# Optimization experiments

Hardware: AMD Instinct MI355X
Metric: run time of the kernel (lower is better)

Reference implementation:

```python
import jax, jax.numpy as jnp
import numpy as np

ND1 = 8000   # block1 num dst nodes
ND2 = 4000   # block2 num dst nodes


def gat_layer(x_src, x_dst, src, dst, num_dst, W, a_src, a_dst, b, heads, ch):
    """PyG GATConv (bipartite tuple input, concat=True) in jax.
    x_src: [B,Ns,F], x_dst: [B,Nd,F]; src/dst: [E] int edge endpoints."""
    B = x_src.shape[0]
    h_s = jnp.einsum('bnf,fk->bnk', x_src, W).reshape(B, -1, heads, ch)  # [B,Ns,H,C]
    h_d = jnp.einsum('bnf,fk->bnk', x_dst, W).reshape(B, -1, heads, ch)  # [B,Nd,H,C]
    e_s = jnp.einsum('bnhc,hc->bnh', h_s, a_src)  # [B,Ns,H]
    e_d = jnp.einsum('bnhc,hc->bnh', h_d, a_dst)  # [B,Nd,H]
    alpha = jax.nn.leaky_relu(e_s[:, src] + e_d[:, dst], 0.2)  # [B,E,H]
    a = jnp.transpose(alpha, (1, 0, 2))  # [E,B,H] (segment ops reduce axis 0)
    amax = jax.ops.segment_max(a, dst, num_segments=num_dst)  # [Nd,B,H]
    ex = jnp.exp(a - amax[dst])
    den = jax.ops.segment_sum(ex, dst, num_segments=num_dst)
    w = ex / (den[dst] + 1e-16)  # edge softmax per (dst,batch,head)
    msg = jnp.transpose(h_s[:, src], (1, 0, 2, 3)) * w[..., None]  # [E,B,H,C]
    out = jax.ops.segment_sum(msg, dst, num_segments=num_dst)  # [Nd,B,H,C]
    out = jnp.transpose(out, (1, 0, 2, 3)).reshape(B, num_dst, heads * ch)
    return out + b


def setup_inputs() -> dict:
    key = jax.random.key(0)
    ks = jax.random.split(key, 16)
    B, N, F = 2, 20000, 128
    E1, E2 = 100000, 60000
    inp = {
        'x': jax.random.normal(ks[0], (B, N, F), jnp.float32),
        'n_id1': jax.random.randint(ks[1], (16000,), 0, N),
        'res_n_id1': jax.random.randint(ks[2], (ND1,), 0, 16000),
        'src1': jax.random.randint(ks[3], (E1,), 0, 16000),
        'dst1': jax.random.randint(ks[4], (E1,), 0, ND1),
        'res_n_id2': jax.random.randint(ks[5], (ND2,), 0, ND1),
        'src2': jax.random.randint(ks[6], (E2,), 0, ND1),
        'dst2': jax.random.randint(ks[7], (E2,), 0, ND2),
        'W1': jax.random.normal(ks[8], (F, 12 * 128), jnp.float32) * 0.05,
        'att_src1': jax.random.normal(ks[9], (12, 128), jnp.float32) * 0.1,
        'att_dst1': jax.random.normal(ks[10], (12, 128), jnp.float32) * 0.1,
        'bias1': jnp.zeros((12 * 128,), jnp.float32),
        'W2': jax.random.normal(ks[11], (12 * 128, 1), jnp.float32) * 0.05,
        'att_src2': jax.random.normal(ks[12], (1, 1), jnp.float32) * 0.1,
        'att_dst2': jax.random.normal(ks[13], (1, 1), jnp.float32) * 0.1,
        'bias2': jnp.zeros((1,), jnp.float32),
    }
    return inp


def reference(x, n_id1, res_n_id1, src1, dst1, res_n_id2, src2, dst2,
              W1, att_src1, att_dst1, bias1, W2, att_src2, att_dst2, bias2):
    # block 1
    xt = x[:, n_id1, :]                       # [B,16000,F]
    xd = xt[:, res_n_id1, :]                  # [B,8000,F]
    h = gat_layer(xt, xd, src1, dst1, ND1, W1, att_src1, att_dst1, bias1, 12, 128)
    h = jax.nn.relu(h)                        # [B,8000,1536]
    # block 2
    hd = h[:, res_n_id2, :]                   # [B,4000,1536]
    out = gat_layer(h, hd, src2, dst2, ND2, W2, att_src2, att_dst2, bias2, 1, 1)
    return out                                # [B,4000,1]
```

## Files before the change

### kernel.cpp

```cpp
#include <hip/hip_runtime.h>
#include <hip/hip_bf16.h>

#define B2      2
#define NX      20000
#define F_IN    128
#define NS1     16000
#define ND1     8000
#define E1      100000
#define ND2     4000
#define E2      60000
#define HEADS   12
#define CH      128
#define K1      1536
#define MROWS   (2*ND1)
#define CAP1    64
#define CAP2    64

typedef __bf16 bf16x8 __attribute__((ext_vector_type(8)));
typedef float  f32x4  __attribute__((ext_vector_type(4)));

static __device__ __forceinline__ float lrelu(float x) { return x > 0.f ? x : 0.2f * x; }

static __device__ __forceinline__ unsigned short f2bf(float f) {
    union { float f; unsigned u; } v; v.f = f;
    unsigned r = v.u + 0x7fffu + ((v.u >> 16) & 1u);
    return (unsigned short)(r >> 16);
}
static __device__ __forceinline__ float bf2f(unsigned short h) {
    union { unsigned u; float f; } v; v.u = ((unsigned)h) << 16;
    return v.f;
}

static __device__ __forceinline__ void gld16(const void* g, void* l) {
    __builtin_amdgcn_global_load_lds(
        (const __attribute__((address_space(1))) unsigned int*)g,
        (__attribute__((address_space(3))) unsigned int*)l, 16, 0, 0);
}

__global__ __launch_bounds__(256) void k_prep(const float* __restrict__ x,
                                              const int* __restrict__ n_id,
                                              const float* __restrict__ W,
                                              const float* __restrict__ asrc,
                                              const float* __restrict__ adst,
                                              unsigned short* __restrict__ xg,
                                              unsigned short* __restrict__ WT,
                                              unsigned short* __restrict__ wswd,
                                              int* __restrict__ dcnt,
                                              float* __restrict__ s2)
{
    const int bx = blockIdx.x;
    const int tid = threadIdx.x;
    if (bx < 4000) {
        int t = bx * 256 + tid;
        int row = t >> 5;
        int c4 = (t & 31) << 2;
        int b = row >= NS1 ? 1 : 0;
        int node = n_id[row - b * NS1];
        const float4 v = *reinterpret_cast<const float4*>(
            x + ((size_t)(b * NX + node)) * F_IN + c4);
        ushort4 o;
        o.x = f2bf(v.x); o.y = f2bf(v.y); o.z = f2bf(v.z); o.w = f2bf(v.w);
        *reinterpret_cast<ushort4*>(xg + (size_t)row * F_IN + c4) = o;
    } else if (bx < 4768) {
        int t = (bx - 4000) * 256 + tid;
        int k = t / K1;
        int n = t - k * K1;
        WT[(size_t)n * F_IN + k] = f2bf(W[t]);
    } else if (bx < 4784) {
        int t = (bx - 4768) * 256 + tid;
        int n = t >> 7;
        int c = t & 127;
        float acc = 0.f;
        if (n < 24) {
            int h = n < 12 ? n : n - 12;
            const float* att = (n < 12 ? asrc : adst) + h * CH;
            const float* wr = W + (size_t)c * K1 + h * CH;
            for (int j = 0; j < CH; ++j) acc += wr[j] * att[j];
        }
        wswd[(size_t)n * F_IN + c] = f2bf(acc);
    } else {
        int t = (bx - 4784) * 256 + tid;
        if (t < ND1 + ND2) dcnt[t] = 0;
        else if (t < ND1 + ND2 + MROWS) s2[t - (ND1 + ND2)] = 0.f;
    }
}

__global__ __launch_bounds__(256) void k_escore(const unsigned short* __restrict__ xg,
                                                const unsigned short* __restrict__ wswd,
                                                float* __restrict__ es,
                                                float* __restrict__ ed)
{
    const int tid = threadIdx.x;
    const int wave = tid >> 6, lane = tid & 63;
    const int l15 = lane & 15, l4 = lane >> 4;
    const int rt = blockIdx.x * 4 + wave;
    const int row0 = rt * 16;
    const unsigned short* Ap = xg + (size_t)(row0 + l15) * F_IN + l4 * 8;

    f32x4 acc[2] = {f32x4{0,0,0,0}, f32x4{0,0,0,0}};
#pragma unroll
    for (int kk = 0; kk < 4; ++kk) {
        bf16x8 a = *reinterpret_cast<const bf16x8*>(Ap + kk * 32);
#pragma unroll
        for (int c = 0; c < 2; ++c) {
            bf16x8 b = *reinterpret_cast<const bf16x8*>(
                wswd + (size_t)(c * 16 + l15) * F_IN + kk * 32 + l4 * 8);
            acc[c] = __builtin_amdgcn_mfma_f32_16x16x32_bf16(a, b, acc[c], 0, 0, 0);
        }
    }
#pragma unroll
    for (int c = 0; c < 2; ++c) {
        int col = c * 16 + l15;
#pragma unroll
        for (int r = 0; r < 4; ++r) {
            int row = row0 + l4 * 4 + r;
            float v = acc[c][r];
            if (col < 12)       es[(size_t)row * HEADS + col] = v;
            else if (col < 24)  ed[(size_t)row * HEADS + (col - 12)] = v;
        }
    }
}

__global__ void k_scatter2(const int* __restrict__ dst1, const int* __restrict__ src1,
                           const int* __restrict__ dst2, const int* __restrict__ src2,
                           const int* __restrict__ res1,
                           const float* __restrict__ es, const float* __restrict__ ed,
                           int* __restrict__ dcnt, unsigned* __restrict__ ew,
                           int* __restrict__ srcp2)
{
    int e = blockIdx.x * 256 + threadIdx.x;
    if (e < E1) {
        int d = dst1[e];
        int k = atomicAdd(&dcnt[d], 1);
        if (k < CAP1) {
            int s = src1[e];
            int rd = res1[d];
#pragma unroll
            for (int b = 0; b < 2; ++b) {
                const float* esp = es + ((size_t)(b * NS1 + s)) * HEADS;
                const float* edp = ed + ((size_t)(b * NS1 + rd)) * HEADS;
                unsigned w[6];
#pragma unroll
                for (int j = 0; j < 6; ++j) {
                    float w0 = __expf(lrelu(esp[2 * j] + edp[2 * j]));
                    float w1 = __expf(lrelu(esp[2 * j + 1] + edp[2 * j + 1]));
                    w[j] = (unsigned)f2bf(w0) | ((unsigned)f2bf(w1) << 16);
                }
                unsigned* rp = ew + ((size_t)b * ND1 * CAP1 + (size_t)d * CAP1 + k) * 8;
                *reinterpret_cast<uint4*>(rp) = make_uint4((unsigned)s, w[0], w[1], w[2]);
                *reinterpret_cast<uint4*>(rp + 4) = make_uint4(w[3], w[4], w[5], 0u);
            }
        }
    } else if (e < E1 + E2) {
        int ee = e - E1;
        int d = dst2[ee];
        int k = atomicAdd(&dcnt[ND1 + d], 1);
        if (k < CAP2) srcp2[d * CAP2 + k] = src2[ee];
    }
}

__global__ __launch_bounds__(256) void k_agg1(const unsigned short* __restrict__ xg,
                                              const unsigned* __restrict__ ew,
                                              const int* __restrict__ dcnt,
                                              unsigned short* __restrict__ agg)
{
    const int tid = threadIdx.x;
    const int wv = tid >> 6, lane = tid & 63;
    const int task = blockIdx.x * 4 + wv;
    const int b = task >= ND1 ? 1 : 0;
    const int i = task - b * ND1;
    const int c2 = lane * 2;

    const int deg = min(dcnt[i], CAP1);
    const uint4* eb = reinterpret_cast<const uint4*>(
        ew + ((size_t)b * ND1 * CAP1 + (size_t)i * CAP1) * 8);
    const unsigned short* xb = xg + (size_t)b * NS1 * F_IN + c2;

    float acc[24];
    float den[12];
#pragma unroll
    for (int r = 0; r < 24; ++r) acc[r] = 0.f;
#pragma unroll
    for (int h = 0; h < 12; ++h) den[h] = 0.f;

#pragma unroll 2
    for (int p = 0; p < deg; ++p) {
        uint4 r0 = eb[2 * p];
        uint4 r1 = eb[2 * p + 1];
        int se = (int)r0.x;
        unsigned xv = *reinterpret_cast<const unsigned*>(xb + (size_t)se * F_IN);
        float x0 = __uint_as_float(xv << 16);
        float x1 = __uint_as_float(xv & 0xffff0000u);
        unsigned wd[6] = {r0.y, r0.z, r0.w, r1.x, r1.y, r1.z};
#pragma unroll
        for (int j = 0; j < 6; ++j) {
            unsigned d = wd[j];
            float w0 = __uint_as_float(d << 16);
            float w1 = __uint_as_float(d & 0xffff0000u);
            acc[4 * j + 0] += w0 * x0; acc[4 * j + 1] += w0 * x1;
            acc[4 * j + 2] += w1 * x0; acc[4 * j + 3] += w1 * x1;
            den[2 * j]     += w0;      den[2 * j + 1] += w1;
        }
    }

    const size_t rowbase = ((size_t)(b * ND1 + i)) * K1;
#pragma unroll
    for (int j = 0; j < 12; ++j) {
        float r = 1.f / (den[j] + 1e-16f);
        unsigned pk = (unsigned)f2bf(acc[2 * j] * r) |
                      ((unsigned)f2bf(acc[2 * j + 1] * r) << 16);
        *reinterpret_cast<unsigned*>(agg + rowbase + j * CH + c2) = pk;
    }
}

__global__ __launch_bounds__(256) void k_out1(const unsigned short* __restrict__ agg,
                                              const unsigned short* __restrict__ WT,
                                              const float* __restrict__ bias1,
                                              const float* __restrict__ W2,
                                              float* __restrict__ s2)
{
    __shared__ unsigned short As[128 * 128];
    __shared__ unsigned short Bs[128 * 128];

    const int tid = threadIdx.x;
    const int wv = tid >> 6, lane = tid & 63;
    const int l15 = lane & 15, l4 = lane >> 4;
    const int row0 = blockIdx.x * 128;
    const int h = blockIdx.y;

    {
        const unsigned short* ga = agg + (size_t)row0 * K1 + h * CH;
        const unsigned short* gb = WT + (size_t)(h * CH) * F_IN;
#pragma unroll
        for (int p = 0; p < 8; ++p) {
            int r = p * 16 + wv * 4 + l4;
            int cs = l15 ^ (r & 7);
            gld16(ga + (size_t)r * K1 + cs * 8, As + (p * 16 + wv * 4) * 128);
            gld16(gb + (size_t)r * F_IN + cs * 8, Bs + (p * 16 + wv * 4) * 128);
        }
    }
    __syncthreads();

    f32x4 acc[2][8];
#pragma unroll
    for (int m = 0; m < 2; ++m)
#pragma unroll
        for (int c = 0; c < 8; ++c) acc[m][c] = f32x4{0, 0, 0, 0};

#pragma unroll
    for (int kk = 0; kk < 4; ++kk) {
        bf16x8 a[2];
#pragma unroll
        for (int m = 0; m < 2; ++m) {
            int r = wv * 32 + m * 16 + l15;
            int ch = (l4 + kk * 4) ^ (r & 7);
            a[m] = *reinterpret_cast<const bf16x8*>(As + r * 128 + ch * 8);
        }
#pragma unroll
        for (int c = 0; c < 8; ++c) {
            int n = c * 16 + l15;
            int ch = (l4 + kk * 4) ^ (n & 7);
            bf16x8 bb = *reinterpret_cast<const bf16x8*>(Bs + n * 128 + ch * 8);
#pragma unroll
            for (int m = 0; m < 2; ++m)
                acc[m][c] = __builtin_amdgcn_mfma_f32_16x16x32_bf16(a[m], bb,
                                                                    acc[m][c], 0, 0, 0);
        }
    }

#pragma unroll
    for (int m = 0; m < 2; ++m) {
        float part[4] = {0.f, 0.f, 0.f, 0.f};
#pragma unroll
        for (int c = 0; c < 8; ++c) {
            int n = h * CH + c * 16 + l15;
            float bi = bias1[n];
            float w2 = W2[n];
#pragma unroll
            for (int r = 0; r < 4; ++r) {
                float v = acc[m][c][r] + bi;
                v = v > 0.f ? v : 0.f;
                part[r] += v * w2;
            }
        }
#pragma unroll
        for (int r = 0; r < 4; ++r) {
#pragma unroll
            for (int o = 1; o < 16; o <<= 1) part[r] += __shfl_xor(part[r], o);
        }
        if (l15 == 0) {
            int row = row0 + wv * 32 + m * 16 + l4 * 4;
#pragma unroll
            for (int r = 0; r < 4; ++r)
                atomicAdd(&s2[row + r], part[r]);
        }
    }
}

__global__ void k_agg2(const float* __restrict__ s2,
                       const int* __restrict__ dcnt2,
                       const int* __restrict__ srcp2,
                       const int* __restrict__ res2,
                       const float* __restrict__ asrc,
                       const float* __restrict__ adst,
                       const float* __restrict__ bias2,
                       float* __restrict__ out)
{
    int t = blockIdx.x * 256 + threadIdx.x;
    if (t >= 2 * ND2) return;
    int b = t / ND2, j = t - b * ND2;
    float a_s = asrc[0], a_d = adst[0];
    float edl = s2[(size_t)b * ND1 + res2[j]] * a_d;
    int deg = min(dcnt2[j], CAP2);
    float den = 0.f, num = 0.f;
    for (int k = 0; k < deg; ++k) {
        int s = srcp2[j * CAP2 + k];
        float v = s2[b * ND1 + s];
        float w = __expf(lrelu(v * a_s + edl));
        den += w;
        num += w * v;
    }
    float o = (deg > 0) ? num / (den + 1e-16f) : 0.f;
    out[(size_t)b * ND2 + j] = o + bias2[0];
}

extern "C" void kernel_launch(void* const* d_in, const int* in_sizes, int n_in,
                              void* d_out, int out_size, void* d_ws, size_t ws_size,
                              hipStream_t stream)
{
    const float* x        = (const float*)d_in[0];
    const int* n_id1      = (const int*)d_in[1];
    const int* res_n_id1  = (const int*)d_in[2];
    const int* src1       = (const int*)d_in[3];
    const int* dst1       = (const int*)d_in[4];
    const int* res_n_id2  = (const int*)d_in[5];
    const int* src2       = (const int*)d_in[6];
    const int* dst2       = (const int*)d_in[7];
    const float* W1       = (const float*)d_in[8];
    const float* att_src1 = (const float*)d_in[9];
    const float* att_dst1 = (const float*)d_in[10];
    const float* bias1    = (const float*)d_in[11];
    const float* W2       = (const float*)d_in[12];
    const float* att_src2 = (const float*)d_in[13];
    const float* att_dst2 = (const float*)d_in[14];
    const float* bias2    = (const float*)d_in[15];

    unsigned short* xg   = (unsigned short*)d_ws;
    unsigned short* W1T  = xg + (size_t)2 * NS1 * F_IN;
    unsigned short* wswd = W1T + (size_t)K1 * F_IN;
    unsigned short* agg  = wswd + (size_t)32 * F_IN;
    float* es  = (float*)(agg + (size_t)2 * ND1 * K1);
    float* ed  = es + (size_t)2 * NS1 * HEADS;
    float* s2  = ed + (size_t)2 * NS1 * HEADS;
    int* dcnt  = (int*)(s2 + (size_t)2 * ND1);
    int* srcp2 = dcnt + (ND1 + ND2);
    unsigned* ew = (unsigned*)(srcp2 + ND2 * CAP2 + 2);
    ew = (unsigned*)(((size_t)ew + 15) & ~(size_t)15);

    k_prep<<<4894, 256, 0, stream>>>(x, n_id1, W1, att_src1, att_dst1,
                                     xg, W1T, wswd, dcnt, s2);

    k_escore<<<500, 256, 0, stream>>>(xg, wswd, es, ed);

    k_scatter2<<<(E1 + E2 + 255) / 256, 256, 0, stream>>>(
        dst1, src1, dst2, src2, res_n_id1, es, ed, dcnt, ew, srcp2);

    k_agg1<<<MROWS / 4, 256, 0, stream>>>(xg, ew, dcnt, agg);

    k_out1<<<dim3(MROWS / 128, HEADS), 256, 0, stream>>>(agg, W1T, bias1, W2, s2);

    k_agg2<<<(2 * ND2 + 255) / 256, 256, 0, stream>>>(s2, dcnt + ND1, srcp2,
                                                      res_n_id2, att_src2,
                                                      att_dst2, bias2,
                                                      (float*)d_out);
}
```

Before: 98.22 us.

## Compute block-1 edge aggregation with MFMA over LDS-staged edge chunks

The per-destination weighted aggregation in k_agg1 is restructured so each wave stages up to 32 edges of weights and gathered source features into LDS, then runs bf16 16x16x32 MFMAs for both the weighted feature sums and the softmax denominators. This replaces the scalar FMA loop, where each lane did 24 multiply-adds plus 12 adds per edge, with matrix-core work. The cost is extra LDS writes, zero-initialisation, shuffles and padding waste for low-degree nodes. Output stores also become 2-byte scattered writes instead of packed 4-byte writes.

```diff
diff --git a/kernel.cpp b/kernel.cpp
--- a/kernel.cpp
+++ b/kernel.cpp
@@ -164,52 +164,119 @@
                                               const int* __restrict__ dcnt,
                                               unsigned short* __restrict__ agg)
 {
+    __shared__ unsigned short Wl[4][16 * 40];
+    __shared__ unsigned short Xl[4][128 * 36];
+
     const int tid = threadIdx.x;
     const int wv = tid >> 6, lane = tid & 63;
+    const int l15 = lane & 15, l4 = lane >> 4;
     const int task = blockIdx.x * 4 + wv;
     const int b = task >= ND1 ? 1 : 0;
     const int i = task - b * ND1;
-    const int c2 = lane * 2;
+
+    unsigned short* Wp = Wl[wv];
+    unsigned short* Xp = Xl[wv];
+
+    {
+        unsigned* wz = reinterpret_cast<unsigned*>(Wp);
+#pragma unroll
+        for (int z = 0; z < 5; ++z) wz[z * 64 + lane] = 0u;
+        unsigned* xz = reinterpret_cast<unsigned*>(Xp);
+#pragma unroll
+        for (int z = 0; z < 36; ++z) xz[z * 64 + lane] = 0u;
+    }
 
     const int deg = min(dcnt[i], CAP1);
     const uint4* eb = reinterpret_cast<const uint4*>(
         ew + ((size_t)b * ND1 * CAP1 + (size_t)i * CAP1) * 8);
-    const unsigned short* xb = xg + (size_t)b * NS1 * F_IN + c2;
-
-    float acc[24];
-    float den[12];
-#pragma unroll
-    for (int r = 0; r < 24; ++r) acc[r] = 0.f;
-#pragma unroll
-    for (int h = 0; h < 12; ++h) den[h] = 0.f;
-
-#pragma unroll 2
-    for (int p = 0; p < deg; ++p) {
-        uint4 r0 = eb[2 * p];
-        uint4 r1 = eb[2 * p + 1];
-        int se = (int)r0.x;
-        unsigned xv = *reinterpret_cast<const unsigned*>(xb + (size_t)se * F_IN);
-        float x0 = __uint_as_float(xv << 16);
-        float x1 = __uint_as_float(xv & 0xffff0000u);
-        unsigned wd[6] = {r0.y, r0.z, r0.w, r1.x, r1.y, r1.z};
-#pragma unroll
-        for (int j = 0; j < 6; ++j) {
-            unsigned d = wd[j];
-            float w0 = __uint_as_float(d << 16);
-            float w1 = __uint_as_float(d & 0xffff0000u);
-            acc[4 * j + 0] += w0 * x0; acc[4 * j + 1] += w0 * x1;
-            acc[4 * j + 2] += w1 * x0; acc[4 * j + 3] += w1 * x1;
-            den[2 * j]     += w0;      den[2 * j + 1] += w1;
+    const unsigned short* xb = xg + (size_t)b * NS1 * F_IN + 2 * lane;
+
+    f32x4 acc[8];
+#pragma unroll
+    for (int c = 0; c < 8; ++c) acc[c] = f32x4{0, 0, 0, 0};
+    f32x4 dacc = f32x4{0, 0, 0, 0};
+
+    bf16x8 ones;
+#pragma unroll
+    for (int j = 0; j < 8; ++j) ones[j] = (__bf16)1.0f;
+
+    const int rr = lane >> 1, hf = lane & 1;
+
+    for (int cb = 0; cb < deg; cb += 32) {
+        const int cnt = min(32, deg - cb);
+
+        uint4 rec = make_uint4(0u, 0u, 0u, 0u);
+        if (rr < cnt) rec = eb[cb * 2 + lane];
+        unsigned d0, d1, d2;
+        int hbase;
+        if (hf == 0) { d0 = rec.y; d1 = rec.z; d2 = rec.w; hbase = 0; }
+        else         { d0 = rec.x; d1 = rec.y; d2 = rec.z; hbase = 6; }
+        int vsrc = (hf == 0) ? (int)rec.x : 0;
+        Wp[(hbase + 0) * 40 + rr] = (unsigned short)(d0 & 0xffffu);
+        Wp[(hbase + 1) * 40 + rr] = (unsigned short)(d0 >> 16);
+        Wp[(hbase + 2) * 40 + rr] = (unsigned short)(d1 & 0xffffu);
+        Wp[(hbase + 3) * 40 + rr] = (unsigned short)(d1 >> 16);
+        Wp[(hbase + 4) * 40 + rr] = (unsigned short)(d2 & 0xffffu);
+        Wp[(hbase + 5) * 40 + rr] = (unsigned short)(d2 >> 16);
+
+        for (int k0 = 0; k0 < cnt; k0 += 4) {
+            unsigned xv0 = 0, xv1 = 0, xv2 = 0, xv3 = 0;
+            {
+                int s0 = __shfl(vsrc, 2 * (k0 + 0));
+                xv0 = *reinterpret_cast<const unsigned*>(xb + (size_t)s0 * F_IN);
+            }
+            if (k0 + 1 < cnt) {
+                int s1 = __shfl(vsrc, 2 * (k0 + 1));
+                xv1 = *reinterpret_cast<const unsigned*>(xb + (size_t)s1 * F_IN);
+            }
+            if (k0 + 2 < cnt) {
+                int s2 = __shfl(vsrc, 2 * (k0 + 2));
+                xv2 = *reinterpret_cast<const unsigned*>(xb + (size_t)s2 * F_IN);
+            }
+            if (k0 + 3 < cnt) {
+                int s3 = __shfl(vsrc, 2 * (k0 + 3));
+                xv3 = *reinterpret_cast<const unsigned*>(xb + (size_t)s3 * F_IN);
+            }
+            Xp[(2 * lane) * 36 + k0]     = (unsigned short)(xv0 & 0xffffu);
+            Xp[(2 * lane + 1) * 36 + k0] = (unsigned short)(xv0 >> 16);
+            if (k0 + 1 < cnt) {
+                Xp[(2 * lane) * 36 + k0 + 1]     = (unsigned short)(xv1 & 0xffffu);
+                Xp[(2 * lane + 1) * 36 + k0 + 1] = (unsigned short)(xv1 >> 16);
+            }
+            if (k0 + 2 < cnt) {
+                Xp[(2 * lane) * 36 + k0 + 2]     = (unsigned short)(xv2 & 0xffffu);
+                Xp[(2 * lane + 1) * 36 + k0 + 2] = (unsigned short)(xv2 >> 16);
+            }
+            if (k0 + 3 < cnt) {
+                Xp[(2 * lane) * 36 + k0 + 3]     = (unsigned short)(xv3 & 0xffffu);
+                Xp[(2 * lane + 1) * 36 + k0 + 3] = (unsigned short)(xv3 >> 16);
+            }
+        }
+
+        bf16x8 aW = *reinterpret_cast<const bf16x8*>(Wp + l15 * 40 + l4 * 8);
+        dacc = __builtin_amdgcn_mfma_f32_16x16x32_bf16(aW, ones, dacc, 0, 0, 0);
+#pragma unroll
+        for (int ct = 0; ct < 8; ++ct) {
+            bf16x8 bX = *reinterpret_cast<const bf16x8*>(
+                Xp + (ct * 16 + l15) * 36 + l4 * 8);
+            acc[ct] = __builtin_amdgcn_mfma_f32_16x16x32_bf16(aW, bX, acc[ct], 0, 0, 0);
         }
     }
 
     const size_t rowbase = ((size_t)(b * ND1 + i)) * K1;
-#pragma unroll
-    for (int j = 0; j < 12; ++j) {
-        float r = 1.f / (den[j] + 1e-16f);
-        unsigned pk = (unsigned)f2bf(acc[2 * j] * r) |
-                      ((unsigned)f2bf(acc[2 * j + 1] * r) << 16);
-        *reinterpret_cast<unsigned*>(agg + rowbase + j * CH + c2) = pk;
+    float rinv[4];
+#pragma unroll
+    for (int q = 0; q < 4; ++q) rinv[q] = 1.f / (dacc[q] + 1e-16f);
+    if (l4 < 3) {
+#pragma unroll
+        for (int ct = 0; ct < 8; ++ct) {
+#pragma unroll
+            for (int q = 0; q < 4; ++q) {
+                int h = l4 * 4 + q;
+                agg[rowbase + (size_t)h * CH + ct * 16 + l15] =
+                    f2bf(acc[ct][q] * rinv[q]);
+            }
+        }
     }
 }
 
```

After: 104.7 us. 6.6% more time.

## Merge six kernels into two persistent cooperative kernels with grid syncs

Applied to the files above, without the earlier changes.

The six stage kernels are refactored into device bodies and run inside two cooperative persistent kernels. Each kernel loops blocks over virtual block indices and uses grid.sync between stages, replacing separate kernel launches and the gaps between them. The risks are reduced occupancy from the launch bounds and grid-stride loops, grid-sync overhead, and host calls for device properties and occupancy on every launch. A fallback to the original per-stage launches is kept.

```diff
diff --git a/kernel.cpp b/kernel.cpp
--- a/kernel.cpp
+++ b/kernel.cpp
@@ -1,5 +1,8 @@
 #include <hip/hip_runtime.h>
 #include <hip/hip_bf16.h>
+#include <hip/hip_cooperative_groups.h>
+
+namespace cg = cooperative_groups;
 
 #define B2      2
 #define NX      20000
@@ -26,10 +29,6 @@
     unsigned r = v.u + 0x7fffu + ((v.u >> 16) & 1u);
     return (unsigned short)(r >> 16);
 }
-static __device__ __forceinline__ float bf2f(unsigned short h) {
-    union { unsigned u; float f; } v; v.u = ((unsigned)h) << 16;
-    return v.f;
-}
 
 static __device__ __forceinline__ void gld16(const void* g, void* l) {
     __builtin_amdgcn_global_load_lds(
@@ -37,19 +36,15 @@
         (__attribute__((address_space(3))) unsigned int*)l, 16, 0, 0);
 }
 
-__global__ __launch_bounds__(256) void k_prep(const float* __restrict__ x,
-                                              const int* __restrict__ n_id,
-                                              const float* __restrict__ W,
-                                              const float* __restrict__ asrc,
-                                              const float* __restrict__ adst,
-                                              unsigned short* __restrict__ xg,
-                                              unsigned short* __restrict__ WT,
-                                              unsigned short* __restrict__ wswd,
-                                              int* __restrict__ dcnt,
-                                              float* __restrict__ s2)
-{
-    const int bx = blockIdx.x;
-    const int tid = threadIdx.x;
+static __device__ __forceinline__ void prep_body(
+        int bx, int tid,
+        const float* __restrict__ x, const int* __restrict__ n_id,
+        const float* __restrict__ W, const float* __restrict__ asrc,
+        const float* __restrict__ adst,
+        unsigned short* __restrict__ xg, unsigned short* __restrict__ WT,
+        unsigned short* __restrict__ wswd,
+        int* __restrict__ dcnt, float* __restrict__ s2)
+{
     if (bx < 4000) {
         int t = bx * 256 + tid;
         int row = t >> 5;
@@ -85,16 +80,15 @@
     }
 }
 
-__global__ __launch_bounds__(256) void k_escore(const unsigned short* __restrict__ xg,
-                                                const unsigned short* __restrict__ wswd,
-                                                float* __restrict__ es,
-                                                float* __restrict__ ed)
-{
-    const int tid = threadIdx.x;
+static __device__ __forceinline__ void escore_body(
+        int vb, int tid,
+        const unsigned short* __restrict__ xg,
+        const unsigned short* __restrict__ wswd,
+        float* __restrict__ es, float* __restrict__ ed)
+{
     const int wave = tid >> 6, lane = tid & 63;
     const int l15 = lane & 15, l4 = lane >> 4;
-    const int rt = blockIdx.x * 4 + wave;
-    const int row0 = rt * 16;
+    const int row0 = (vb * 4 + wave) * 16;
     const unsigned short* Ap = xg + (size_t)(row0 + l15) * F_IN + l4 * 8;
 
     f32x4 acc[2] = {f32x4{0,0,0,0}, f32x4{0,0,0,0}};
@@ -121,14 +115,15 @@
     }
 }
 
-__global__ void k_scatter2(const int* __restrict__ dst1, const int* __restrict__ src1,
-                           const int* __restrict__ dst2, const int* __restrict__ src2,
-                           const int* __restrict__ res1,
-                           const float* __restrict__ es, const float* __restrict__ ed,
-                           int* __restrict__ dcnt, unsigned* __restrict__ ew,
-                           int* __restrict__ srcp2)
-{
-    int e = blockIdx.x * 256 + threadIdx.x;
+static __device__ __forceinline__ void scatter_body(
+        int e,
+        const int* __restrict__ dst1, const int* __restrict__ src1,
+        const int* __restrict__ dst2, const int* __restrict__ src2,
+        const int* __restrict__ res1,
+        const float* __restrict__ es, const float* __restrict__ ed,
+        int* __restrict__ dcnt, unsigned* __restrict__ ew,
+        int* __restrict__ srcp2)
+{
     if (e < E1) {
         int d = dst1[e];
         int k = atomicAdd(&dcnt[d], 1);
@@ -159,14 +154,15 @@
     }
 }
 
-__global__ __launch_bounds__(256) void k_agg1(const unsigned short* __restrict__ xg,
-                                              const unsigned* __restrict__ ew,
-                                              const int* __restrict__ dcnt,
-                                              unsigned short* __restrict__ agg)
-{
-    const int tid = threadIdx.x;
+static __device__ __forceinline__ void agg1_body(
+        int vb, int tid,
+        const unsigned short* __restrict__ xg,
+        const unsigned* __restrict__ ew,
+        const int* __restrict__ dcnt,
+        unsigned short* __restrict__ agg)
+{
     const int wv = tid >> 6, lane = tid & 63;
-    const int task = blockIdx.x * 4 + wv;
+    const int task = vb * 4 + wv;
     const int b = task >= ND1 ? 1 : 0;
     const int i = task - b * ND1;
     const int c2 = lane * 2;
@@ -213,20 +209,16 @@
     }
 }
 
-__global__ __launch_bounds__(256) void k_out1(const unsigned short* __restrict__ agg,
-                                              const unsigned short* __restrict__ WT,
-                                              const float* __restrict__ bias1,
-                                              const float* __restrict__ W2,
-                                              float* __restrict__ s2)
-{
-    __shared__ unsigned short As[128 * 128];
-    __shared__ unsigned short Bs[128 * 128];
-
-    const int tid = threadIdx.x;
+static __device__ __forceinline__ void out1_body(
+        int vb, int tid, unsigned short* As, unsigned short* Bs,
+        const unsigned short* __restrict__ agg, const unsigned short* __restrict__ WT,
+        const float* __restrict__ bias1, const float* __restrict__ W2,
+        float* __restrict__ s2)
+{
     const int wv = tid >> 6, lane = tid & 63;
     const int l15 = lane & 15, l4 = lane >> 4;
-    const int row0 = blockIdx.x * 128;
-    const int h = blockIdx.y;
+    const int h = vb / 125;
+    const int row0 = (vb - h * 125) * 128;
 
     {
         const unsigned short* ga = agg + (size_t)row0 * K1 + h * CH;
@@ -295,18 +287,16 @@
                 atomicAdd(&s2[row + r], part[r]);
         }
     }
-}
-
-__global__ void k_agg2(const float* __restrict__ s2,
-                       const int* __restrict__ dcnt2,
-                       const int* __restrict__ srcp2,
-                       const int* __restrict__ res2,
-                       const float* __restrict__ asrc,
-                       const float* __restrict__ adst,
-                       const float* __restrict__ bias2,
-                       float* __restrict__ out)
-{
-    int t = blockIdx.x * 256 + threadIdx.x;
+    __syncthreads();
+}
+
+static __device__ __forceinline__ void agg2_body(
+        int t,
+        const float* __restrict__ s2, const int* __restrict__ dcnt2,
+        const int* __restrict__ srcp2, const int* __restrict__ res2,
+        const float* __restrict__ asrc, const float* __restrict__ adst,
+        const float* __restrict__ bias2, float* __restrict__ out)
+{
     if (t >= 2 * ND2) return;
     int b = t / ND2, j = t - b * ND2;
     float a_s = asrc[0], a_d = adst[0];
@@ -322,6 +312,122 @@
     }
     float o = (deg > 0) ? num / (den + 1e-16f) : 0.f;
     out[(size_t)b * ND2 + j] = o + bias2[0];
+}
+
+__global__ __launch_bounds__(256, 4) void k_coopA(
+        const float* __restrict__ x, const int* __restrict__ n_id,
+        const float* __restrict__ W, const float* __restrict__ asrc,
+        const float* __restrict__ adst,
+        const int* __restrict__ src1, const int* __restrict__ dst1,
+        const int* __restrict__ src2, const int* __restrict__ dst2,
+        const int* __restrict__ res1,
+        unsigned short* __restrict__ xg, unsigned short* __restrict__ WT,
+        unsigned short* __restrict__ wswd,
+        int* __restrict__ dcnt, float* __restrict__ s2,
+        float* __restrict__ es, float* __restrict__ ed,
+        unsigned* __restrict__ ew, int* __restrict__ srcp2,
+        unsigned short* __restrict__ agg)
+{
+    cg::grid_group grid = cg::this_grid();
+    const int tid = threadIdx.x;
+    const int nb = gridDim.x;
+
+    for (int bx = blockIdx.x; bx < 4894; bx += nb)
+        prep_body(bx, tid, x, n_id, W, asrc, adst, xg, WT, wswd, dcnt, s2);
+    grid.sync();
+
+    for (int vb = blockIdx.x; vb < 500; vb += nb)
+        escore_body(vb, tid, xg, wswd, es, ed);
+    grid.sync();
+
+    for (int vb = blockIdx.x; vb < 625; vb += nb)
+        scatter_body(vb * 256 + tid, dst1, src1, dst2, src2, res1,
+                     es, ed, dcnt, ew, srcp2);
+    grid.sync();
+
+    for (int vb = blockIdx.x; vb < MROWS / 4; vb += nb)
+        agg1_body(vb, tid, xg, ew, dcnt, agg);
+}
+
+__global__ __launch_bounds__(256, 2) void k_coopB(
+        const unsigned short* __restrict__ agg, const unsigned short* __restrict__ WT,
+        const float* __restrict__ bias1, const float* __restrict__ W2,
+        float* __restrict__ s2,
+        const int* __restrict__ dcnt2, const int* __restrict__ srcp2,
+        const int* __restrict__ res2, const float* __restrict__ asrc2,
+        const float* __restrict__ adst2, const float* __restrict__ bias2,
+        float* __restrict__ out)
+{
+    cg::grid_group grid = cg::this_grid();
+    __shared__ unsigned short As[128 * 128];
+    __shared__ unsigned short Bs[128 * 128];
+    const int tid = threadIdx.x;
+
+    for (int vb = blockIdx.x; vb < 125 * HEADS; vb += gridDim.x)
+        out1_body(vb, tid, As, Bs, agg, WT, bias1, W2, s2);
+    grid.sync();
+
+    for (int vb = blockIdx.x; vb < (2 * ND2 + 255) / 256; vb += gridDim.x)
+        agg2_body(vb * 256 + tid, s2, dcnt2, srcp2, res2, asrc2, adst2,
+                  bias2, out);
+}
+
+__global__ __launch_bounds__(256) void k_prep(
+        const float* __restrict__ x, const int* __restrict__ n_id,
+        const float* __restrict__ W, const float* __restrict__ asrc,
+        const float* __restrict__ adst,
+        unsigned short* __restrict__ xg, unsigned short* __restrict__ WT,
+        unsigned short* __restrict__ wswd,
+        int* __restrict__ dcnt, float* __restrict__ s2)
+{
+    prep_body(blockIdx.x, threadIdx.x, x, n_id, W, asrc, adst, xg, WT, wswd,
+              dcnt, s2);
+}
+
+__global__ __launch_bounds__(256) void k_escore(
+        const unsigned short* __restrict__ xg,
+        const unsigned short* __restrict__ wswd,
+        float* __restrict__ es, float* __restrict__ ed)
+{
+    escore_body(blockIdx.x, threadIdx.x, xg, wswd, es, ed);
+}
+
+__global__ void k_scatter2(const int* __restrict__ dst1, const int* __restrict__ src1,
+                           const int* __restrict__ dst2, const int* __restrict__ src2,
+                           const int* __restrict__ res1,
+                           const float* __restrict__ es, const float* __restrict__ ed,
+                           int* __restrict__ dcnt, unsigned* __restrict__ ew,
+                           int* __restrict__ srcp2)
+{
+    scatter_body(blockIdx.x * 256 + threadIdx.x, dst1, src1, dst2, src2, res1,
+                 es, ed, dcnt, ew, srcp2);
+}
+
+__global__ __launch_bounds__(256) void k_agg1(
+        const unsigned short* __restrict__ xg, const unsigned* __restrict__ ew,
+        const int* __restrict__ dcnt, unsigned short* __restrict__ agg)
+{
+    agg1_body(blockIdx.x, threadIdx.x, xg, ew, dcnt, agg);
+}
+
+__global__ __launch_bounds__(256) void k_out1(
+        const unsigned short* __restrict__ agg, const unsigned short* __restrict__ WT,
+        const float* __restrict__ bias1, const float* __restrict__ W2,
+        float* __restrict__ s2)
+{
+    __shared__ unsigned short As[128 * 128];
+    __shared__ unsigned short Bs[128 * 128];
+    int vb = blockIdx.y * 125 + blockIdx.x;
+    out1_body(vb, threadIdx.x, As, Bs, agg, WT, bias1, W2, s2);
+}
+
+__global__ void k_agg2(const float* __restrict__ s2, const int* __restrict__ dcnt2,
+                       const int* __restrict__ srcp2, const int* __restrict__ res2,
+                       const float* __restrict__ asrc, const float* __restrict__ adst,
+                       const float* __restrict__ bias2, float* __restrict__ out)
+{
+    agg2_body(blockIdx.x * 256 + threadIdx.x, s2, dcnt2, srcp2, res2, asrc,
+              adst, bias2, out);
 }
 
 extern "C" void kernel_launch(void* const* d_in, const int* in_sizes, int n_in,
@@ -356,21 +462,59 @@
     int* srcp2 = dcnt + (ND1 + ND2);
     unsigned* ew = (unsigned*)(srcp2 + ND2 * CAP2 + 2);
     ew = (unsigned*)(((size_t)ew + 15) & ~(size_t)15);
-
-    k_prep<<<4894, 256, 0, stream>>>(x, n_id1, W1, att_src1, att_dst1,
-                                     xg, W1T, wswd, dcnt, s2);
-
-    k_escore<<<500, 256, 0, stream>>>(xg, wswd, es, ed);
-
-    k_scatter2<<<(E1 + E2 + 255) / 256, 256, 0, stream>>>(
-        dst1, src1, dst2, src2, res_n_id1, es, ed, dcnt, ew, srcp2);
-
-    k_agg1<<<MROWS / 4, 256, 0, stream>>>(xg, ew, dcnt, agg);
-
-    k_out1<<<dim3(MROWS / 128, HEADS), 256, 0, stream>>>(agg, W1T, bias1, W2, s2);
-
-    k_agg2<<<(2 * ND2 + 255) / 256, 256, 0, stream>>>(s2, dcnt + ND1, srcp2,
-                                                      res_n_id2, att_src2,
-                                                      att_dst2, bias2,
-                                                      (float*)d_out);
-}
+    int* dcnt2 = dcnt + ND1;
+    float* outp = (float*)d_out;
+
+    int nCU = 256;
+    {
+        hipDeviceProp_t prop;
+        if (hipGetDeviceProperties(&prop, 0) == hipSuccess && prop.multiProcessorCount > 0)
+            nCU = prop.multiProcessorCount;
+    }
+    int occA = 0, occB = 0;
+    hipOccupancyMaxActiveBlocksPerMultiprocessor(&occA, (const void*)k_coopA, 256, 0);
+    hipOccupancyMaxActiveBlocksPerMultiprocessor(&occB, (const void*)k_coopB, 256, 0);
+    if (occA > 4) occA = 4;
+    if (occB > 2) occB = 2;
+
+    bool a_done = false, b_done = false;
+
+    if (occA >= 1) {
+        int gridA = occA * nCU;
+        void* args[] = {
+            (void*)&x, (void*)&n_id1, (void*)&W1, (void*)&att_src1, (void*)&att_dst1,
+            (void*)&src1, (void*)&dst1, (void*)&src2, (void*)&dst2, (void*)&res_n_id1,
+            (void*)&xg, (void*)&W1T, (void*)&wswd,
+            (void*)&dcnt, (void*)&s2, (void*)&es, (void*)&ed,
+            (void*)&ew, (void*)&srcp2, (void*)&agg
+        };
+        if (hipLaunchCooperativeKernel((const void*)k_coopA, dim3(gridA), dim3(256),
+                                       args, 0, stream) == hipSuccess)
+            a_done = true;
+    }
+    if (!a_done) {
+        k_prep<<<4894, 256, 0, stream>>>(x, n_id1, W1, att_src1, att_dst1,
+                                         xg, W1T, wswd, dcnt, s2);
+        k_escore<<<500, 256, 0, stream>>>(xg, wswd, es, ed);
+        k_scatter2<<<(E1 + E2 + 255) / 256, 256, 0, stream>>>(
+            dst1, src1, dst2, src2, res_n_id1, es, ed, dcnt, ew, srcp2);
+        k_agg1<<<MROWS / 4, 256, 0, stream>>>(xg, ew, dcnt, agg);
+    }
+
+    if (occB >= 1) {
+        int gridB = occB * nCU;
+        void* args[] = {
+            (void*)&agg, (void*)&W1T, (void*)&bias1, (void*)&W2,
+            (void*)&s2, (void*)&dcnt2, (void*)&srcp2, (void*)&res_n_id2,
+            (void*)&att_src2, (void*)&att_dst2, (void*)&bias2, (void*)&outp
+        };
+        if (hipLaunchCooperativeKernel((const void*)k_coopB, dim3(gridB), dim3(256),
+                                       args, 0, stream) == hipSuccess)
+            b_done = true;
+    }
+    if (!b_done) {
+        k_out1<<<dim3(125, HEADS), 256, 0, stream>>>(agg, W1T, bias1, W2, s2);
+        k_agg2<<<(2 * ND2 + 255) / 256, 256, 0, stream>>>(
+            s2, dcnt2, srcp2, res_n_id2, att_src2, att_dst2, bias2, outp);
+    }
+}
```

New measurement: 369.9 us. 277% more time.
